# Kernel optimization log

Hardware: AMD Instinct MI355X
Metric: run time of the kernel (lower is better)

The kernel has to match this reference:

```python
import jax, jax.numpy as jnp
import numpy as np

N_NODES = 100000
N_EDGES = 1600000
HIDDEN = 64
LEAKY_SLOPE = 0.01  # torch F.leaky_relu default


def setup_inputs() -> dict:
    key = jax.random.key(0)
    k1, k2, k3, k4 = jax.random.split(key, 4)
    x = jax.random.normal(k1, (N_NODES, HIDDEN), dtype=jnp.float32)
    edge_index = jax.random.randint(k2, (2, N_EDGES), 0, N_NODES, dtype=jnp.int64)
    # Linear(hidden, 1, bias=False) weights, squeezed to [hidden]
    w_i = jax.random.normal(k3, (HIDDEN,), dtype=jnp.float32) * 0.1
    w_j = jax.random.normal(k4, (HIDDEN,), dtype=jnp.float32) * 0.1
    return {"x": x, "edge_index": edge_index, "w_i": w_i, "w_j": w_j}


def reference(x, edge_index, w_i, w_j):
    n = x.shape[0]
    ej, ei = edge_index[0], edge_index[1]  # (edge_index_j, edge_index_i)
    # per-node attention scores, then per-edge gather
    s_i = x @ w_i  # [N]
    s_j = x @ w_j  # [N]
    e = jax.nn.leaky_relu(s_i[ei] + s_j[ej], LEAKY_SLOPE)  # [E]
    # segment softmax over edges grouped by destination node ei
    emax = jax.ops.segment_max(e, ei, num_segments=n)  # [N]
    ex = jnp.exp(e - emax[ei])  # [E]
    denom = jax.ops.segment_sum(ex, ei, num_segments=n)  # [N]
    alpha = ex / denom[ei]  # [E]
    # spmm: out[i] = sum_{edges e: dst=i} alpha_e * x[src_e]
    out = jax.ops.segment_sum(alpha[:, None] * x[ej], ei, num_segments=n)  # [N, H]
    return jax.nn.relu(out)
```

## Files before the change

kernel.cpp:

```cpp
#include <hip/hip_runtime.h>
#include <stdint.h>

#define N_NODES 100000
#define N_EDGES 1600000
#define HIDDEN  64
#define SLOPE   0.01f
#define NBUCK   782
#define CAPB    2816
#define PCHUNK  4096
#define NPART   391
#define NSB     1563
#define NAGG    3125
#define NCAP    48


__device__ __forceinline__ unsigned short f2bf(float f) {
    uint32_t u = __float_as_uint(f);
    uint32_t r = u + 0x7FFFu + ((u >> 16) & 1u);
    return (unsigned short)(r >> 16);
}

__global__ void __launch_bounds__(256) k_build(const float* __restrict__ x,
                                               const float* __restrict__ w_i,
                                               const float* __restrict__ w_j,
                                               const int* __restrict__ srcs,
                                               const int* __restrict__ dsts,
                                               float* __restrict__ s_i,
                                               float* __restrict__ s_j,
                                               unsigned short* __restrict__ xb,
                                               int* __restrict__ ctrl,
                                               uint32_t* __restrict__ pairs) {
    __shared__ int lcnt[NBUCK], lbase[NBUCK];
    int tid = threadIdx.x;
    if (blockIdx.x < NPART) {
        if (blockIdx.x == 0) {
            for (int i = tid; i < NBUCK; i += 256) atomicExch(&ctrl[i], 0);
            __syncthreads();
            if (tid == 0) { __threadfence(); atomicExch(&ctrl[NBUCK], 1); }
        }
        for (int b = tid; b < NBUCK; b += 256) lcnt[b] = 0;
        __syncthreads();
        int e0 = blockIdx.x * PCHUNK;
        int e1 = min(e0 + PCHUNK, N_EDGES);
        for (int e = e0 + tid; e < e1; e += 256)
            atomicAdd(&lcnt[dsts[e] >> 7], 1);
        if (tid == 0)
            while (atomicAdd(&ctrl[NBUCK], 0) != 1) {}
        __syncthreads();
        for (int b = tid; b < NBUCK; b += 256) {
            int c = lcnt[b];
            lbase[b] = c ? atomicAdd(&ctrl[b], c) : 0;
            lcnt[b] = 0;
        }
        __syncthreads();
        for (int e = e0 + tid; e < e1; e += 256) {
            int src = srcs[e];
            int dst = dsts[e];
            int b = dst >> 7;
            int r = atomicAdd(&lcnt[b], 1);
            int pos = lbase[b] + r;
            if (pos < CAPB)
                pairs[(size_t)b * CAPB + pos] =
                    ((uint32_t)(dst & 127) << 24) | (uint32_t)src;
        }
        return;
    }
    int u0 = blockIdx.x - NPART;
    int wave = tid >> 6, lane = tid & 63;
    int sub = lane >> 4, ql = lane & 15;
    float4 wi4 = ((const float4*)w_i)[ql];
    float4 wj4 = ((const float4*)w_j)[ql];
#pragma unroll
    for (int i = 0; i < 4; ++i) {
        int node = u0 * 64 + i * 16 + wave * 4 + sub;
        if (node >= N_NODES) break;
        float4 v = ((const float4*)x)[node * 16 + ql];
        float a = v.x * wi4.x + v.y * wi4.y + v.z * wi4.z + v.w * wi4.w;
        float b = v.x * wj4.x + v.y * wj4.y + v.z * wj4.z + v.w * wj4.w;
#pragma unroll
        for (int off = 1; off < 16; off <<= 1) {
            a += __shfl_xor(a, off, 64);
            b += __shfl_xor(b, off, 64);
        }
        if (ql == 0) { s_i[node] = a; s_j[node] = b; }
        ushort4 o;
        o.x = f2bf(v.x); o.y = f2bf(v.y); o.z = f2bf(v.z); o.w = f2bf(v.w);
        ((ushort4*)xb)[node * 16 + ql] = o;
    }
}

__device__ __forceinline__ float bflo(uint32_t d) { return __uint_as_float(d << 16); }
__device__ __forceinline__ float bfhi(uint32_t d) { return __uint_as_float(d & 0xFFFF0000u); }

template <int L>
__device__ __forceinline__ void gat_batch4(const uint64_t* pp, int i, int quarter, int ql,
                                           const uint2* __restrict__ xw2,
                                           float acc[4], float& den) {
    uint64_t q[L];
    uint2 d[L];
#pragma unroll
    for (int t = 0; t < L; ++t) q[t] = pp[i + 4 * t + quarter];
#pragma unroll
    for (int t = 0; t < L; ++t)
        d[t] = xw2[((uint32_t)q[t] & 0xFFFFFFu) * 16 + ql];
#pragma unroll
    for (int t = 0; t < L; ++t) {
        float w = __uint_as_float((uint32_t)(q[t] >> 32));
        den += w;
        acc[0] = fmaf(w, bflo(d[t].x), acc[0]);
        acc[1] = fmaf(w, bfhi(d[t].x), acc[1]);
        acc[2] = fmaf(w, bflo(d[t].y), acc[2]);
        acc[3] = fmaf(w, bfhi(d[t].y), acc[3]);
    }
}

__global__ void __launch_bounds__(256, 8) k_bucket_agg(const uint2* __restrict__ xw2,
                                                       const uint32_t* __restrict__ pairs,
                                                       const int* __restrict__ ctrl,
                                                       const float* __restrict__ s_i,
                                                       const float* __restrict__ s_j,
                                                       float* __restrict__ out) {
    __shared__ uint64_t spairs[32 * NCAP];
    __shared__ int lcur[32];
    __shared__ float s_si[32];
    int tid = threadIdx.x;
    int g = blockIdx.x;
    int cb = g >> 2, sub = g & 3;
    int node0 = g * 32;
    const uint32_t* reg = pairs + (size_t)cb * CAPB;
    int rcnt = min(ctrl[cb], CAPB);
    if (tid < 32) {
        lcur[tid] = 0;
        int node = node0 + tid;
        s_si[tid] = (node < N_NODES) ? s_i[node] : 0.f;
    }
    __syncthreads();
    for (int e = tid; e < rcnt; e += 256) {
        uint32_t p = reg[e];
        int dstl = (int)(p >> 24);
        if ((dstl >> 5) == sub) {
            int n = dstl & 31;
            int src = (int)(p & 0xFFFFFFu);
            float sc = s_si[n] + s_j[src];
            sc = (sc > 0.f) ? sc : SLOPE * sc;
            float w = __expf(sc);
            int slot = atomicAdd(&lcur[n], 1);
            if (slot < NCAP)
                spairs[n * NCAP + slot] =
                    ((uint64_t)__float_as_uint(w) << 32) | (uint32_t)src;
        }
    }
    __syncthreads();
    int wave = tid >> 6, lane = tid & 63;
    int quarter = lane >> 4, ql = lane & 15;
    for (int k = wave; k < 32; k += 4) {
        int node = node0 + k;
        if (node >= N_NODES) break;
        float acc[4] = {0.f, 0.f, 0.f, 0.f};
        float den = 0.f;
        int c = lcur[k];
        if (c <= NCAP) {
            const uint64_t* pp = spairs + k * NCAP;
            int i = 0;
            for (; i + 16 <= c; i += 16) gat_batch4<4>(pp, i, quarter, ql, xw2, acc, den);
            if (i + 8 <= c) { gat_batch4<2>(pp, i, quarter, ql, xw2, acc, den); i += 8; }
            if (i + 4 <= c) { gat_batch4<1>(pp, i, quarter, ql, xw2, acc, den); i += 4; }
            int rem = c - i;
            if (rem > 0) {
                uint64_t q = pp[i + min(quarter, rem - 1)];
                float w = (quarter < rem) ? __uint_as_float((uint32_t)(q >> 32)) : 0.f;
                uint2 d = xw2[((uint32_t)q & 0xFFFFFFu) * 16 + ql];
                den += w;
                acc[0] = fmaf(w, bflo(d.x), acc[0]);
                acc[1] = fmaf(w, bfhi(d.x), acc[1]);
                acc[2] = fmaf(w, bflo(d.y), acc[2]);
                acc[3] = fmaf(w, bfhi(d.y), acc[3]);
            }
        } else {
            int sn = (sub << 5) | k;
            for (int e = 0; e < rcnt; ++e) {
                uint32_t p = reg[e];
                if ((int)(p >> 24) == sn) {
                    int src = (int)(p & 0xFFFFFFu);
                    float sc = s_si[k] + s_j[src];
                    sc = (sc > 0.f) ? sc : SLOPE * sc;
                    float w = (quarter == 0) ? __expf(sc) : 0.f;
                    uint2 d = xw2[(uint32_t)src * 16 + ql];
                    den += w;
                    acc[0] = fmaf(w, bflo(d.x), acc[0]);
                    acc[1] = fmaf(w, bfhi(d.x), acc[1]);
                    acc[2] = fmaf(w, bflo(d.y), acc[2]);
                    acc[3] = fmaf(w, bfhi(d.y), acc[3]);
                }
            }
        }
#pragma unroll
        for (int j = 0; j < 4; ++j) {
            acc[j] += __shfl_xor(acc[j], 16, 64);
            acc[j] += __shfl_xor(acc[j], 32, 64);
        }
        den += __shfl_xor(den, 16, 64);
        den += __shfl_xor(den, 32, 64);
        if (quarter == 0) {
            float4 r = make_float4(0.f, 0.f, 0.f, 0.f);
            if (c > 0) {
                float inv = 1.f / den;
                r.x = fmaxf(acc[0] * inv, 0.f);
                r.y = fmaxf(acc[1] * inv, 0.f);
                r.z = fmaxf(acc[2] * inv, 0.f);
                r.w = fmaxf(acc[3] * inv, 0.f);
            }
            ((float4*)(out + (size_t)node * HIDDEN))[ql] = r;
        }
    }
}

extern "C" void kernel_launch(void* const* d_in, const int* in_sizes, int n_in,
                              void* d_out, int out_size, void* d_ws, size_t ws_size,
                              hipStream_t stream) {
    const float* x   = (const float*)d_in[0];
    const int*   ei  = (const int*)d_in[1];
    const float* w_i = (const float*)d_in[2];
    const float* w_j = (const float*)d_in[3];
    float* out = (float*)d_out;

    char* p = (char*)d_ws;
    float*          s_i   = (float*)p;          p += (size_t)N_NODES * 4;
    float*          s_j   = (float*)p;          p += (size_t)N_NODES * 4;
    unsigned short* xb    = (unsigned short*)p; p += (size_t)N_NODES * HIDDEN * 2;
    int*            ctrl  = (int*)p;            p += 4096;
    uint32_t*       pairs = (uint32_t*)p;

    const int* srcs = ei;
    const int* dsts = ei + N_EDGES;

    k_build     <<<NPART + NSB, 256, 0, stream>>>(x, w_i, w_j, srcs, dsts,
                                                  s_i, s_j, xb, ctrl, pairs);
    k_bucket_agg<<<NAGG, 256, 0, stream>>>((const uint2*)xb, pairs, ctrl,
                                           s_i, s_j, out);
}
```

Measured before the change: 156.1 us.

## Stage bucket partition in shared memory and scatter contiguous runs with larger blocks

The partition phase now uses 1024-thread blocks over 16K-edge chunks, which cuts the number of global atomics on the bucket counters. It computes local bucket offsets with a block scan and sorts records into shared memory first. Each wave then writes contiguous runs per bucket to global memory instead of scattering every record on its own, aiming for more coalesced writes. The cost is a long serial scan with many syncthreads, 64KB+ of shared memory per block that limits occupancy, and fewer partition blocks (98) to spread across the CUs. The node-score part is remapped to cover 256 nodes per 1024-thread block.

```diff
diff --git a/kernel.cpp b/kernel.cpp
--- a/kernel.cpp
+++ b/kernel.cpp
@@ -7,9 +7,9 @@
 #define SLOPE   0.01f
 #define NBUCK   782
 #define CAPB    2816
-#define PCHUNK  4096
-#define NPART   391
-#define NSB     1563
+#define PCHUNK  16384
+#define NPART   98
+#define NSB     391
 #define NAGG    3125
 #define NCAP    48
 
@@ -20,59 +20,79 @@
     return (unsigned short)(r >> 16);
 }
 
-__global__ void __launch_bounds__(256) k_build(const float* __restrict__ x,
-                                               const float* __restrict__ w_i,
-                                               const float* __restrict__ w_j,
-                                               const int* __restrict__ srcs,
-                                               const int* __restrict__ dsts,
-                                               float* __restrict__ s_i,
-                                               float* __restrict__ s_j,
-                                               unsigned short* __restrict__ xb,
-                                               int* __restrict__ ctrl,
-                                               uint32_t* __restrict__ pairs) {
-    __shared__ int lcnt[NBUCK], lbase[NBUCK];
+__global__ void __launch_bounds__(1024) k_build(const float* __restrict__ x,
+                                                const float* __restrict__ w_i,
+                                                const float* __restrict__ w_j,
+                                                const int* __restrict__ srcs,
+                                                const int* __restrict__ dsts,
+                                                float* __restrict__ s_i,
+                                                float* __restrict__ s_j,
+                                                unsigned short* __restrict__ xb,
+                                                int* __restrict__ ctrl,
+                                                uint32_t* __restrict__ pairs) {
+    __shared__ int lcnt[NBUCK], lloc[NBUCK], lbase[NBUCK];
+    __shared__ int scan[1024];
+    __shared__ uint32_t srec[PCHUNK];
     int tid = threadIdx.x;
     if (blockIdx.x < NPART) {
         if (blockIdx.x == 0) {
-            for (int i = tid; i < NBUCK; i += 256) atomicExch(&ctrl[i], 0);
+            if (tid < NBUCK) atomicExch(&ctrl[tid], 0);
             __syncthreads();
             if (tid == 0) { __threadfence(); atomicExch(&ctrl[NBUCK], 1); }
         }
-        for (int b = tid; b < NBUCK; b += 256) lcnt[b] = 0;
+        if (tid < NBUCK) lcnt[tid] = 0;
         __syncthreads();
         int e0 = blockIdx.x * PCHUNK;
         int e1 = min(e0 + PCHUNK, N_EDGES);
-        for (int e = e0 + tid; e < e1; e += 256)
+        for (int e = e0 + tid; e < e1; e += 1024)
             atomicAdd(&lcnt[dsts[e] >> 7], 1);
+        __syncthreads();
+        int v = (tid < NBUCK) ? lcnt[tid] : 0;
+        scan[tid] = v;
+        __syncthreads();
+        for (int off = 1; off < 1024; off <<= 1) {
+            int t = (tid >= off) ? scan[tid - off] : 0;
+            __syncthreads();
+            scan[tid] += t;
+            __syncthreads();
+        }
+        if (tid < NBUCK) lloc[tid] = scan[tid] - v;
         if (tid == 0)
             while (atomicAdd(&ctrl[NBUCK], 0) != 1) {}
         __syncthreads();
-        for (int b = tid; b < NBUCK; b += 256) {
-            int c = lcnt[b];
-            lbase[b] = c ? atomicAdd(&ctrl[b], c) : 0;
-            lcnt[b] = 0;
-        }
-        __syncthreads();
-        for (int e = e0 + tid; e < e1; e += 256) {
+        if (tid < NBUCK) {
+            lbase[tid] = v ? atomicAdd(&ctrl[tid], v) : 0;
+            lcnt[tid] = 0;
+        }
+        __syncthreads();
+        for (int e = e0 + tid; e < e1; e += 1024) {
             int src = srcs[e];
             int dst = dsts[e];
             int b = dst >> 7;
             int r = atomicAdd(&lcnt[b], 1);
-            int pos = lbase[b] + r;
-            if (pos < CAPB)
-                pairs[(size_t)b * CAPB + pos] =
-                    ((uint32_t)(dst & 127) << 24) | (uint32_t)src;
+            srec[lloc[b] + r] = ((uint32_t)(dst & 127) << 24) | (uint32_t)src;
+        }
+        __syncthreads();
+        int wv = tid >> 6, ln = tid & 63;
+        for (int b = wv; b < NBUCK; b += 16) {
+            int c = lcnt[b];
+            int lo = lloc[b], go = lbase[b];
+            for (int j = ln; j < c; j += 64) {
+                int pos = go + j;
+                if (pos < CAPB)
+                    pairs[(size_t)b * CAPB + pos] = srec[lo + j];
+            }
         }
         return;
     }
     int u0 = blockIdx.x - NPART;
-    int wave = tid >> 6, lane = tid & 63;
-    int sub = lane >> 4, ql = lane & 15;
+    int g16 = tid >> 4;
+    int ql = tid & 15;
     float4 wi4 = ((const float4*)w_i)[ql];
     float4 wj4 = ((const float4*)w_j)[ql];
 #pragma unroll
     for (int i = 0; i < 4; ++i) {
-        int node = u0 * 64 + i * 16 + wave * 4 + sub;
+        int node = u0 * 256 + i * 64 + g16;
         if (node >= N_NODES) break;
         float4 v = ((const float4*)x)[node * 16 + ql];
         float a = v.x * wi4.x + v.y * wi4.y + v.z * wi4.z + v.w * wi4.w;
@@ -234,8 +254,8 @@
     const int* srcs = ei;
     const int* dsts = ei + N_EDGES;
 
-    k_build     <<<NPART + NSB, 256, 0, stream>>>(x, w_i, w_j, srcs, dsts,
-                                                  s_i, s_j, xb, ctrl, pairs);
+    k_build     <<<NPART + NSB, 1024, 0, stream>>>(x, w_i, w_j, srcs, dsts,
+                                                   s_i, s_j, xb, ctrl, pairs);
     k_bucket_agg<<<NAGG, 256, 0, stream>>>((const uint2*)xb, pairs, ctrl,
                                            s_i, s_j, out);
 }
```

Result: faster. 150.4 us (-3.6%).
